# Optimization experiments

Hardware: AMD Instinct MI355X
Metric: run time of the kernel (lower is better)

The kernel has to match this reference:

```python
import jax, jax.numpy as jnp
import numpy as np

B, D_IN, D_H, W_RANK, U_RANK = 8192, 1024, 2048, 256, 256


def setup_inputs() -> dict:
    key = jax.random.key(0)
    ks = jax.random.split(key, 6)
    return {
        "input": jax.random.normal(ks[0], (B, D_IN), dtype=jnp.float32),
        "state": jax.random.normal(ks[1], (B, D_H), dtype=jnp.float32),
        "W1": 0.1 * jax.random.normal(ks[2], (W_RANK, D_IN), dtype=jnp.float32),
        "W2": 0.1 * jax.random.normal(ks[3], (D_H, W_RANK), dtype=jnp.float32),
        "U1": 0.1 * jax.random.normal(ks[4], (U_RANK, D_H), dtype=jnp.float32),
        "U2": 0.1 * jax.random.normal(ks[5], (D_H, U_RANK), dtype=jnp.float32),
        "bias_gate": jnp.ones((1, D_H), dtype=jnp.float32),
        "bias_update": jnp.ones((1, D_H), dtype=jnp.float32),
        "zeta": 1.0 * jnp.ones((1, 1), dtype=jnp.float32),
        "nu": -4.0 * jnp.ones((1, 1), dtype=jnp.float32),
    }


def reference(input, state, W1, W2, U1, U2, bias_gate, bias_update, zeta, nu):
    # Low-rank projections: Wx = x @ W1^T @ W2^T ; Uh = h @ U1^T @ U2^T
    wx = jnp.einsum("bi,ri->br", input, W1)          # [B, wRank]
    wx = jnp.einsum("br,hr->bh", wx, W2)             # [B, H]
    uh = jnp.einsum("bh,rh->br", state, U1)          # [B, uRank]
    uh = jnp.einsum("br,hr->bh", uh, U2)             # [B, H]
    pre = wx + uh                                     # shared pre-activation
    z = jax.nn.sigmoid(pre + bias_gate)               # gate (sigmoid)
    h_cand = jnp.tanh(pre + bias_update)              # update (tanh)
    # h_t = z*h_{t-1} + (sigmoid(zeta)*(1-z) + sigmoid(nu)) * h_cand
    new_h = z * state + (jax.nn.sigmoid(zeta) * (1.0 - z) + jax.nn.sigmoid(nu)) * h_cand
    return new_h
```

## Files before the change

kernel.cpp:

```cpp
#include <hip/hip_runtime.h>
#include <hip/hip_fp16.h>
#include <cstdint>
#include <cstddef>


typedef _Float16 half8 __attribute__((ext_vector_type(8)));
typedef float f32x4 __attribute__((ext_vector_type(4)));

#define DIN 1024
#define DH 2048
#define RK 256
#define RB6LD 1536
#define OFF_W1H 0
#define OFF_U1H 262144
#define OFF_W2H 786432
#define OFF_U2H 1310720
#define WB_HALVES 1835008

__device__ __forceinline__ half8 cvt8(const float4 a, const float4 b) {
  half8 h;
  h[0] = (_Float16)a.x; h[1] = (_Float16)a.y; h[2] = (_Float16)a.z; h[3] = (_Float16)a.w;
  h[4] = (_Float16)b.x; h[5] = (_Float16)b.y; h[6] = (_Float16)b.z; h[7] = (_Float16)b.w;
  return h;
}

__global__ __launch_bounds__(256)
void fgrnn_prep(const float* __restrict__ W1, const float* __restrict__ U1,
                const float* __restrict__ W2, const float* __restrict__ U2,
                _Float16* __restrict__ wb) {
  const int q = blockIdx.x * 256 + threadIdx.x;
  const float* src;
  int rel;
  if (q < 65536) { src = W1; rel = q; }
  else if (q < 196608) { src = U1; rel = q - 65536; }
  else if (q < 327680) { src = W2; rel = q - 196608; }
  else { src = U2; rel = q - 327680; }
  const float4 v = reinterpret_cast<const float4*>(src)[rel];
  union { _Float16 h[4]; uint2 u; } cv;
  cv.h[0] = (_Float16)v.x; cv.h[1] = (_Float16)v.y;
  cv.h[2] = (_Float16)v.z; cv.h[3] = (_Float16)v.w;
  reinterpret_cast<uint2*>(wb)[q] = cv.u;
}

__global__ __launch_bounds__(256)
void fgrnn_stage1(const float* __restrict__ x, const float* __restrict__ h,
                  const _Float16* __restrict__ wb, _Float16* __restrict__ rb6) {
  const int bid = blockIdx.x;
  const int L = (bid & 7) * 192 + (bid >> 3);
  const int p = L >> 8;
  const int rem = L & 255;
  const int ncol = rem >> 7;
  const int mtile = rem & 127;
  const bool isx = (p < 2);
  const float* A = isx ? x : h;
  const int KA = isx ? DIN : DH;
  const int kbase = (isx ? p : (p - 2)) * 512;
  const _Float16* Bw = wb + (isx ? OFF_W1H : OFF_U1H) + (size_t)(ncol * 128) * KA;
  const int row0 = mtile * 64;
  const int colbase = p * 256 + ncol * 128;

  __shared__ _Float16 As[64 * 64];
  __shared__ _Float16 Bs[128 * 64];

  const int tid = threadIdx.x;
  const int lane = tid & 63;
  const int w = tid >> 6;
  const int wr = w >> 1, wc = w & 1;

  f32x4 acc[2][4];
#pragma unroll
  for (int i = 0; i < 2; ++i)
#pragma unroll
    for (int j = 0; j < 4; ++j) acc[i][j] = (f32x4){0.f, 0.f, 0.f, 0.f};

  const int sr = tid >> 3;
  const int sc = (tid & 7) * 8;

  float4 pa4[2][2];
  half8 pb[4];

  auto LOADG = [&](int it) {
    const int k0 = kbase + it * 64;
#pragma unroll
    for (int j = 0; j < 2; ++j) {
      const float* s = A + (size_t)(row0 + j * 32 + sr) * KA + k0 + sc;
      pa4[j][0] = *reinterpret_cast<const float4*>(s);
      pa4[j][1] = *reinterpret_cast<const float4*>(s + 4);
    }
#pragma unroll
    for (int j = 0; j < 4; ++j)
      pb[j] = *reinterpret_cast<const half8*>(Bw + (size_t)(j * 32 + sr) * KA + k0 + sc);
  };
  auto STORE = [&]() {
#pragma unroll
    for (int j = 0; j < 2; ++j) {
      const int r = j * 32 + sr;
      *reinterpret_cast<half8*>(&As[r * 64 + (sc ^ ((r & 7) << 3))]) =
          cvt8(pa4[j][0], pa4[j][1]);
    }
#pragma unroll
    for (int j = 0; j < 4; ++j) {
      const int r = j * 32 + sr;
      *reinterpret_cast<half8*>(&Bs[r * 64 + (sc ^ ((r & 7) << 3))]) = pb[j];
    }
  };

  LOADG(0);
  STORE();
  __syncthreads();

  for (int it = 0; it < 8; ++it) {
    const bool more = (it + 1 < 8);
    if (more) LOADG(it + 1);
#pragma unroll
    for (int kk = 0; kk < 64; kk += 32) {
      half8 af[2], bf[4];
#pragma unroll
      for (int mi = 0; mi < 2; ++mi) {
        const int r = wr * 32 + mi * 16 + (lane & 15);
        af[mi] = *reinterpret_cast<const half8*>(
            &As[r * 64 + ((kk + 8 * (lane >> 4)) ^ ((r & 7) << 3))]);
      }
#pragma unroll
      for (int ni = 0; ni < 4; ++ni) {
        const int r = wc * 64 + ni * 16 + (lane & 15);
        bf[ni] = *reinterpret_cast<const half8*>(
            &Bs[r * 64 + ((kk + 8 * (lane >> 4)) ^ ((r & 7) << 3))]);
      }
#pragma unroll
      for (int mi = 0; mi < 2; ++mi)
#pragma unroll
        for (int ni = 0; ni < 4; ++ni)
          acc[mi][ni] =
              __builtin_amdgcn_mfma_f32_16x16x32_f16(af[mi], bf[ni], acc[mi][ni], 0, 0, 0);
    }
    if (more) {
      __syncthreads();
      STORE();
    }
    __syncthreads();
  }

#pragma unroll
  for (int mi = 0; mi < 2; ++mi)
#pragma unroll
    for (int ni = 0; ni < 4; ++ni)
#pragma unroll
      for (int e = 0; e < 4; ++e) {
        const int row = row0 + wr * 32 + mi * 16 + 4 * (lane >> 4) + e;
        const int col = colbase + wc * 64 + ni * 16 + (lane & 15);
        rb6[(size_t)row * RB6LD + col] = (_Float16)acc[mi][ni][e];
      }
}

__global__ __launch_bounds__(256)
void fgrnn_reduce(const _Float16* __restrict__ rb6, _Float16* __restrict__ rb2) {
  const int t = blockIdx.x * 256 + threadIdx.x;
  const int row = t >> 6;
  const int ch = t & 63;
  const _Float16* src = rb6 + (size_t)row * RB6LD;
  half8 s;
  int outcol;
  if (ch < 32) {
    const int c = ch * 8;
    s = *reinterpret_cast<const half8*>(src + c) +
        *reinterpret_cast<const half8*>(src + 256 + c);
    outcol = c;
  } else {
    const int c = (ch - 32) * 8;
    const _Float16* su = src + 512;
    s = *reinterpret_cast<const half8*>(su + c) +
        *reinterpret_cast<const half8*>(su + 256 + c);
    s = s + *reinterpret_cast<const half8*>(su + 512 + c);
    s = s + *reinterpret_cast<const half8*>(su + 768 + c);
    outcol = 256 + c;
  }
  *reinterpret_cast<half8*>(rb2 + (size_t)row * 512 + outcol) = s;
}

__global__ __launch_bounds__(256)
void fgrnn_stage2(const _Float16* __restrict__ rb2, const _Float16* __restrict__ wb,
                  const float* __restrict__ state,
                  const float* __restrict__ bg, const float* __restrict__ bu,
                  const float* __restrict__ zeta, const float* __restrict__ nu,
                  float* __restrict__ out) {
  const int bid = blockIdx.x;
  const int L = (bid & 7) * 256 + (bid >> 3);
  const int mtile = L >> 4;
  const int ntile = L & 15;
  const int row0 = mtile * 64;
  const int col0 = ntile * 128;
  const _Float16* W2h = wb + OFF_W2H;
  const _Float16* U2h = wb + OFF_U2H;

  __shared__ _Float16 As[64 * 64];
  __shared__ _Float16 Bs[128 * 64];

  const int tid = threadIdx.x;
  const int lane = tid & 63;
  const int w = tid >> 6;
  const int wr = w >> 1, wc = w & 1;

  f32x4 acc[2][4];
#pragma unroll
  for (int i = 0; i < 2; ++i)
#pragma unroll
    for (int j = 0; j < 4; ++j) acc[i][j] = (f32x4){0.f, 0.f, 0.f, 0.f};

  const int sr = tid >> 3;
  const int sc = (tid & 7) * 8;

  half8 pa[2], pb[4];

  auto LOADG = [&](int it) {
    const int k0 = it * 64;
#pragma unroll
    for (int j = 0; j < 2; ++j)
      pa[j] = *reinterpret_cast<const half8*>(rb2 + (size_t)(row0 + j * 32 + sr) * 512 + k0 + sc);
    const _Float16* Bh = (k0 < 256) ? W2h : U2h;
    const int kb = k0 & 255;
#pragma unroll
    for (int j = 0; j < 4; ++j)
      pb[j] = *reinterpret_cast<const half8*>(Bh + (size_t)(col0 + j * 32 + sr) * RK + kb + sc);
  };
  auto STORE = [&]() {
#pragma unroll
    for (int j = 0; j < 2; ++j) {
      const int r = j * 32 + sr;
      *reinterpret_cast<half8*>(&As[r * 64 + (sc ^ ((r & 7) << 3))]) = pa[j];
    }
#pragma unroll
    for (int j = 0; j < 4; ++j) {
      const int r = j * 32 + sr;
      *reinterpret_cast<half8*>(&Bs[r * 64 + (sc ^ ((r & 7) << 3))]) = pb[j];
    }
  };

  LOADG(0);
  STORE();
  __syncthreads();

  for (int it = 0; it < 8; ++it) {
    const bool more = (it + 1 < 8);
    if (more) LOADG(it + 1);
#pragma unroll
    for (int kk = 0; kk < 64; kk += 32) {
      half8 af[2], bf[4];
#pragma unroll
      for (int mi = 0; mi < 2; ++mi) {
        const int r = wr * 32 + mi * 16 + (lane & 15);
        af[mi] = *reinterpret_cast<const half8*>(
            &As[r * 64 + ((kk + 8 * (lane >> 4)) ^ ((r & 7) << 3))]);
      }
#pragma unroll
      for (int ni = 0; ni < 4; ++ni) {
        const int r = wc * 64 + ni * 16 + (lane & 15);
        bf[ni] = *reinterpret_cast<const half8*>(
            &Bs[r * 64 + ((kk + 8 * (lane >> 4)) ^ ((r & 7) << 3))]);
      }
#pragma unroll
      for (int mi = 0; mi < 2; ++mi)
#pragma unroll
        for (int ni = 0; ni < 4; ++ni)
          acc[mi][ni] =
              __builtin_amdgcn_mfma_f32_16x16x32_f16(af[mi], bf[ni], acc[mi][ni], 0, 0, 0);
    }
    if (more) {
      __syncthreads();
      STORE();
    }
    __syncthreads();
  }

  const float LOG2E = 1.44269504f;
  const float sz = __builtin_amdgcn_rcpf(1.f + __builtin_amdgcn_exp2f(-zeta[0] * LOG2E));
  const float sn = __builtin_amdgcn_rcpf(1.f + __builtin_amdgcn_exp2f(-nu[0] * LOG2E));
#pragma unroll
  for (int mi = 0; mi < 2; ++mi)
#pragma unroll
    for (int ni = 0; ni < 4; ++ni) {
      const int col = col0 + wc * 64 + ni * 16 + (lane & 15);
      const float bgc = bg[col];
      const float buc = bu[col];
#pragma unroll
      for (int e = 0; e < 4; ++e) {
        const int row = row0 + wr * 32 + mi * 16 + 4 * (lane >> 4) + e;
        const float pre = acc[mi][ni][e];
        const float zg =
            __builtin_amdgcn_rcpf(1.f + __builtin_amdgcn_exp2f(-(pre + bgc) * LOG2E));
        const float hc =
            1.f - 2.f * __builtin_amdgcn_rcpf(
                            1.f + __builtin_amdgcn_exp2f((pre + buc) * (2.f * LOG2E)));
        const float sv = state[(size_t)row * DH + col];
        out[(size_t)row * DH + col] = zg * sv + (sz * (1.f - zg) + sn) * hc;
      }
    }
}

extern "C" void kernel_launch(void* const* d_in, const int* in_sizes, int n_in,
                              void* d_out, int out_size, void* d_ws, size_t ws_size,
                              hipStream_t stream) {
  const float* input = (const float*)d_in[0];
  const float* state = (const float*)d_in[1];
  const float* W1 = (const float*)d_in[2];
  const float* W2 = (const float*)d_in[3];
  const float* U1 = (const float*)d_in[4];
  const float* U2 = (const float*)d_in[5];
  const float* bg = (const float*)d_in[6];
  const float* bu = (const float*)d_in[7];
  const float* zeta = (const float*)d_in[8];
  const float* nu = (const float*)d_in[9];
  float* out = (float*)d_out;

  _Float16* rb6 = (_Float16*)d_ws;
  _Float16* rb2 = rb6 + (size_t)8192 * RB6LD;
  _Float16* wb = rb2 + (size_t)8192 * 512;

  fgrnn_prep<<<1792, 256, 0, stream>>>(W1, U1, W2, U2, wb);
  fgrnn_stage1<<<1536, 256, 0, stream>>>(input, state, wb, rb6);
  fgrnn_reduce<<<2048, 256, 0, stream>>>(rb6, rb2);
  fgrnn_stage2<<<2048, 256, 0, stream>>>(rb2, wb, state, bg, bu, zeta, nu, out);
}
```

Before: 85.75 us.

## Use direct global-to-LDS loads with triple-buffered pipeline in stage1 GEMM

Stage1 now fetches A (fp32) and B (fp16) tiles straight into shared memory with global_load_lds, using three buffers and a K-step of 32 instead of a register-staged double buffer with K-step 64. The fp32-to-fp16 conversion of A moves from the store phase to the LDS-read phase inside compute. Waits use explicit vmcnt counts, and MFMA sections run at raised priority. The goal is to overlap memory latency with MFMA work and cut register pressure and barrier overhead. In exchange, A takes twice the LDS space and bandwidth as fp32, there are twice as many iterations, and the hand-counted vmcnt waits are fragile.

```diff
diff --git a/kernel.cpp b/kernel.cpp
--- a/kernel.cpp
+++ b/kernel.cpp
@@ -15,13 +15,24 @@
 #define OFF_U1H 262144
 #define OFF_W2H 786432
 #define OFF_U2H 1310720
-#define WB_HALVES 1835008
-
+
+__device__ __forceinline__ half8 cvt8f(f32x4 a, f32x4 b) {
+  half8 h;
+  h[0] = (_Float16)a[0]; h[1] = (_Float16)a[1]; h[2] = (_Float16)a[2]; h[3] = (_Float16)a[3];
+  h[4] = (_Float16)b[0]; h[5] = (_Float16)b[1]; h[6] = (_Float16)b[2]; h[7] = (_Float16)b[3];
+  return h;
+}
 __device__ __forceinline__ half8 cvt8(const float4 a, const float4 b) {
   half8 h;
   h[0] = (_Float16)a.x; h[1] = (_Float16)a.y; h[2] = (_Float16)a.z; h[3] = (_Float16)a.w;
   h[4] = (_Float16)b.x; h[5] = (_Float16)b.y; h[6] = (_Float16)b.z; h[7] = (_Float16)b.w;
   return h;
+}
+
+__device__ __forceinline__ void gload16(const void* g, void* lds) {
+  __builtin_amdgcn_global_load_lds(
+      (const __attribute__((address_space(1))) unsigned*)g,
+      (__attribute__((address_space(3))) unsigned*)lds, 16, 0, 0);
 }
 
 __global__ __launch_bounds__(256)
@@ -45,6 +56,9 @@
 __global__ __launch_bounds__(256)
 void fgrnn_stage1(const float* __restrict__ x, const float* __restrict__ h,
                   const _Float16* __restrict__ wb, _Float16* __restrict__ rb6) {
+  __shared__ float Af[3][64 * 32];
+  __shared__ _Float16 Bf[3][128 * 32];
+
   const int bid = blockIdx.x;
   const int L = (bid & 7) * 192 + (bid >> 3);
   const int p = L >> 8;
@@ -59,13 +73,10 @@
   const int row0 = mtile * 64;
   const int colbase = p * 256 + ncol * 128;
 
-  __shared__ _Float16 As[64 * 64];
-  __shared__ _Float16 Bs[128 * 64];
-
   const int tid = threadIdx.x;
   const int lane = tid & 63;
-  const int w = tid >> 6;
-  const int wr = w >> 1, wc = w & 1;
+  const int wv = tid >> 6;
+  const int wr = wv >> 1, wc = wv & 1;
 
   f32x4 acc[2][4];
 #pragma unroll
@@ -73,72 +84,72 @@
 #pragma unroll
     for (int j = 0; j < 4; ++j) acc[i][j] = (f32x4){0.f, 0.f, 0.f, 0.f};
 
-  const int sr = tid >> 3;
-  const int sc = (tid & 7) * 8;
-
-  float4 pa4[2][2];
-  half8 pb[4];
-
-  auto LOADG = [&](int it) {
-    const int k0 = kbase + it * 64;
-#pragma unroll
-    for (int j = 0; j < 2; ++j) {
-      const float* s = A + (size_t)(row0 + j * 32 + sr) * KA + k0 + sc;
-      pa4[j][0] = *reinterpret_cast<const float4*>(s);
-      pa4[j][1] = *reinterpret_cast<const float4*>(s + 4);
-    }
-#pragma unroll
-    for (int j = 0; j < 4; ++j)
-      pb[j] = *reinterpret_cast<const half8*>(Bw + (size_t)(j * 32 + sr) * KA + k0 + sc);
+  const int aRowL = (lane >> 3);
+  const int aCh = (lane & 7) ^ aRowL;
+  const int bRowL = (lane >> 2);
+  const int bCh = (lane & 3) ^ (lane >> 4);
+
+  auto GLOAD = [&](int buf, int it) {
+    const int k0 = kbase + it * 32;
+#pragma unroll
+    for (int g = 0; g < 2; ++g) {
+      const int rb = wv * 16 + g * 8;
+      gload16(A + (size_t)(row0 + rb + aRowL) * KA + k0 + aCh * 4,
+              &Af[buf][rb * 32]);
+    }
+#pragma unroll
+    for (int g = 0; g < 2; ++g) {
+      const int rb = wv * 32 + g * 16;
+      gload16(Bw + (size_t)(rb + bRowL) * KA + k0 + bCh * 8,
+              &Bf[buf][rb * 32]);
+    }
   };
-  auto STORE = [&]() {
-#pragma unroll
-    for (int j = 0; j < 2; ++j) {
-      const int r = j * 32 + sr;
-      *reinterpret_cast<half8*>(&As[r * 64 + (sc ^ ((r & 7) << 3))]) =
-          cvt8(pa4[j][0], pa4[j][1]);
-    }
-#pragma unroll
-    for (int j = 0; j < 4; ++j) {
-      const int r = j * 32 + sr;
-      *reinterpret_cast<half8*>(&Bs[r * 64 + (sc ^ ((r & 7) << 3))]) = pb[j];
-    }
+
+  auto COMPUTE = [&](int buf) {
+    half8 af[2], bf[4];
+    const int g = lane >> 4;
+#pragma unroll
+    for (int mi = 0; mi < 2; ++mi) {
+      const int r = wr * 32 + mi * 16 + (lane & 15);
+      const int c0 = (2 * g) ^ (r & 7);
+      const int c1 = (2 * g + 1) ^ (r & 7);
+      const f32x4 lo = *reinterpret_cast<const f32x4*>(&Af[buf][r * 32 + c0 * 4]);
+      const f32x4 hi = *reinterpret_cast<const f32x4*>(&Af[buf][r * 32 + c1 * 4]);
+      af[mi] = cvt8f(lo, hi);
+    }
+#pragma unroll
+    for (int ni = 0; ni < 4; ++ni) {
+      const int r = wc * 64 + ni * 16 + (lane & 15);
+      const int c = g ^ ((r >> 2) & 3);
+      bf[ni] = *reinterpret_cast<const half8*>(&Bf[buf][r * 32 + c * 8]);
+    }
+#pragma unroll
+    for (int mi = 0; mi < 2; ++mi)
+#pragma unroll
+      for (int ni = 0; ni < 4; ++ni)
+        acc[mi][ni] =
+            __builtin_amdgcn_mfma_f32_16x16x32_f16(af[mi], bf[ni], acc[mi][ni], 0, 0, 0);
   };
 
-  LOADG(0);
-  STORE();
-  __syncthreads();
-
-  for (int it = 0; it < 8; ++it) {
-    const bool more = (it + 1 < 8);
-    if (more) LOADG(it + 1);
-#pragma unroll
-    for (int kk = 0; kk < 64; kk += 32) {
-      half8 af[2], bf[4];
-#pragma unroll
-      for (int mi = 0; mi < 2; ++mi) {
-        const int r = wr * 32 + mi * 16 + (lane & 15);
-        af[mi] = *reinterpret_cast<const half8*>(
-            &As[r * 64 + ((kk + 8 * (lane >> 4)) ^ ((r & 7) << 3))]);
-      }
-#pragma unroll
-      for (int ni = 0; ni < 4; ++ni) {
-        const int r = wc * 64 + ni * 16 + (lane & 15);
-        bf[ni] = *reinterpret_cast<const half8*>(
-            &Bs[r * 64 + ((kk + 8 * (lane >> 4)) ^ ((r & 7) << 3))]);
-      }
-#pragma unroll
-      for (int mi = 0; mi < 2; ++mi)
-#pragma unroll
-        for (int ni = 0; ni < 4; ++ni)
-          acc[mi][ni] =
-              __builtin_amdgcn_mfma_f32_16x16x32_f16(af[mi], bf[ni], acc[mi][ni], 0, 0, 0);
-    }
-    if (more) {
-      __syncthreads();
-      STORE();
-    }
-    __syncthreads();
+  GLOAD(0, 0);
+  GLOAD(1, 1);
+  asm volatile("s_waitcnt vmcnt(4)" ::: "memory");
+  __builtin_amdgcn_s_barrier();
+  __builtin_amdgcn_sched_barrier(0);
+
+#pragma unroll
+  for (int t = 0; t < 16; ++t) {
+    if (t + 2 < 16) GLOAD((t + 2) % 3, t + 2);
+    __builtin_amdgcn_s_setprio(1);
+    COMPUTE(t % 3);
+    __builtin_amdgcn_s_setprio(0);
+    if (t + 2 < 16) {
+      asm volatile("s_waitcnt vmcnt(4)" ::: "memory");
+    } else if (t + 1 < 16) {
+      asm volatile("s_waitcnt vmcnt(0)" ::: "memory");
+    }
+    __builtin_amdgcn_s_barrier();
+    __builtin_amdgcn_sched_barrier(0);
   }
 
 #pragma unroll
```

Result: no change. 85.96 us (+0.2%).

## Preload whole A row-panel into LDS and double-buffer B tiles in stage1

Applied to the files above, without the earlier changes.

Stage1 now uses 32-row M tiles instead of 64, doubling the grid to 3072 blocks. Each block converts its full 32x512 A slice to fp16 in LDS up front, and only the B tiles are streamed through a double-buffered LDS pipeline. The aim is more parallelism and less per-iteration global traffic and conversion work for A. In exchange, each B tile is reloaded by twice as many blocks, each wave does half as much MFMA work per B fragment read, and LDS use per block grows to about 64KB, which may cap occupancy.

```diff
diff --git a/kernel.cpp b/kernel.cpp
--- a/kernel.cpp
+++ b/kernel.cpp
@@ -15,7 +15,6 @@
 #define OFF_U1H 262144
 #define OFF_W2H 786432
 #define OFF_U2H 1310720
-#define WB_HALVES 1835008
 
 __device__ __forceinline__ half8 cvt8(const float4 a, const float4 b) {
   half8 h;
@@ -45,112 +44,102 @@
 __global__ __launch_bounds__(256)
 void fgrnn_stage1(const float* __restrict__ x, const float* __restrict__ h,
                   const _Float16* __restrict__ wb, _Float16* __restrict__ rb6) {
+  __shared__ _Float16 Ap[32 * 512];
+  __shared__ _Float16 Bs[2][128 * 64];
+
   const int bid = blockIdx.x;
-  const int L = (bid & 7) * 192 + (bid >> 3);
-  const int p = L >> 8;
-  const int rem = L & 255;
-  const int ncol = rem >> 7;
-  const int mtile = rem & 127;
+  const int L = (bid & 7) * 384 + (bid >> 3);
+  const int p = L / 512;
+  const int rem = L & 511;
+  const int ncol = rem >> 8;
+  const int mtile = rem & 255;
   const bool isx = (p < 2);
   const float* A = isx ? x : h;
   const int KA = isx ? DIN : DH;
   const int kbase = (isx ? p : (p - 2)) * 512;
   const _Float16* Bw = wb + (isx ? OFF_W1H : OFF_U1H) + (size_t)(ncol * 128) * KA;
-  const int row0 = mtile * 64;
+  const int row0 = mtile * 32;
   const int colbase = p * 256 + ncol * 128;
-
-  __shared__ _Float16 As[64 * 64];
-  __shared__ _Float16 Bs[128 * 64];
 
   const int tid = threadIdx.x;
   const int lane = tid & 63;
-  const int w = tid >> 6;
-  const int wr = w >> 1, wc = w & 1;
-
-  f32x4 acc[2][4];
-#pragma unroll
-  for (int i = 0; i < 2; ++i)
-#pragma unroll
-    for (int j = 0; j < 4; ++j) acc[i][j] = (f32x4){0.f, 0.f, 0.f, 0.f};
+  const int wv = tid >> 6;
+  const int wr = wv >> 1, wc = wv & 1;
+
+  {
+    const int ar = tid >> 3;
+    const int ac0 = (tid & 7) * 8;
+    const float* src = A + (size_t)(row0 + ar) * KA + kbase;
+#pragma unroll
+    for (int pass = 0; pass < 8; ++pass) {
+      const int c = ac0 + pass * 64;
+      const float4 v0 = *reinterpret_cast<const float4*>(src + c);
+      const float4 v1 = *reinterpret_cast<const float4*>(src + c + 4);
+      const int ch = (c >> 3) ^ (ar & 7);
+      *reinterpret_cast<half8*>(&Ap[ar * 512 + ch * 8]) = cvt8(v0, v1);
+    }
+  }
 
   const int sr = tid >> 3;
   const int sc = (tid & 7) * 8;
-
-  float4 pa4[2][2];
   half8 pb[4];
-
-  auto LOADG = [&](int it) {
+  auto LOADB = [&](int it) {
     const int k0 = kbase + it * 64;
-#pragma unroll
-    for (int j = 0; j < 2; ++j) {
-      const float* s = A + (size_t)(row0 + j * 32 + sr) * KA + k0 + sc;
-      pa4[j][0] = *reinterpret_cast<const float4*>(s);
-      pa4[j][1] = *reinterpret_cast<const float4*>(s + 4);
-    }
 #pragma unroll
     for (int j = 0; j < 4; ++j)
       pb[j] = *reinterpret_cast<const half8*>(Bw + (size_t)(j * 32 + sr) * KA + k0 + sc);
   };
-  auto STORE = [&]() {
-#pragma unroll
-    for (int j = 0; j < 2; ++j) {
-      const int r = j * 32 + sr;
-      *reinterpret_cast<half8*>(&As[r * 64 + (sc ^ ((r & 7) << 3))]) =
-          cvt8(pa4[j][0], pa4[j][1]);
-    }
+  auto STOREB = [&](int buf) {
 #pragma unroll
     for (int j = 0; j < 4; ++j) {
       const int r = j * 32 + sr;
-      *reinterpret_cast<half8*>(&Bs[r * 64 + (sc ^ ((r & 7) << 3))]) = pb[j];
+      *reinterpret_cast<half8*>(&Bs[buf][r * 64 + (sc ^ ((r & 7) << 3))]) = pb[j];
     }
   };
 
-  LOADG(0);
-  STORE();
+  f32x4 acc[4];
+#pragma unroll
+  for (int j = 0; j < 4; ++j) acc[j] = (f32x4){0.f, 0.f, 0.f, 0.f};
+
+  LOADB(0);
+  STOREB(0);
   __syncthreads();
 
   for (int it = 0; it < 8; ++it) {
     const bool more = (it + 1 < 8);
-    if (more) LOADG(it + 1);
+    const int buf = it & 1;
+    if (more) LOADB(it + 1);
 #pragma unroll
     for (int kk = 0; kk < 64; kk += 32) {
-      half8 af[2], bf[4];
-#pragma unroll
-      for (int mi = 0; mi < 2; ++mi) {
-        const int r = wr * 32 + mi * 16 + (lane & 15);
-        af[mi] = *reinterpret_cast<const half8*>(
-            &As[r * 64 + ((kk + 8 * (lane >> 4)) ^ ((r & 7) << 3))]);
+      const int r = wr * 16 + (lane & 15);
+      const int chA = (it * 8 + (kk >> 3) + (lane >> 4)) ^ (r & 7);
+      const half8 af = *reinterpret_cast<const half8*>(&Ap[r * 512 + chA * 8]);
+      half8 bf[4];
+#pragma unroll
+      for (int ni = 0; ni < 4; ++ni) {
+        const int rb_ = wc * 64 + ni * 16 + (lane & 15);
+        bf[ni] = *reinterpret_cast<const half8*>(
+            &Bs[buf][rb_ * 64 + ((kk + 8 * (lane >> 4)) ^ ((rb_ & 7) << 3))]);
       }
 #pragma unroll
-      for (int ni = 0; ni < 4; ++ni) {
-        const int r = wc * 64 + ni * 16 + (lane & 15);
-        bf[ni] = *reinterpret_cast<const half8*>(
-            &Bs[r * 64 + ((kk + 8 * (lane >> 4)) ^ ((r & 7) << 3))]);
-      }
-#pragma unroll
-      for (int mi = 0; mi < 2; ++mi)
-#pragma unroll
-        for (int ni = 0; ni < 4; ++ni)
-          acc[mi][ni] =
-              __builtin_amdgcn_mfma_f32_16x16x32_f16(af[mi], bf[ni], acc[mi][ni], 0, 0, 0);
+      for (int ni = 0; ni < 4; ++ni)
+        acc[ni] = __builtin_amdgcn_mfma_f32_16x16x32_f16(af, bf[ni], acc[ni], 0, 0, 0);
     }
     if (more) {
       __syncthreads();
-      STORE();
+      STOREB(buf ^ 1);
     }
     __syncthreads();
   }
 
 #pragma unroll
-  for (int mi = 0; mi < 2; ++mi)
-#pragma unroll
-    for (int ni = 0; ni < 4; ++ni)
-#pragma unroll
-      for (int e = 0; e < 4; ++e) {
-        const int row = row0 + wr * 32 + mi * 16 + 4 * (lane >> 4) + e;
-        const int col = colbase + wc * 64 + ni * 16 + (lane & 15);
-        rb6[(size_t)row * RB6LD + col] = (_Float16)acc[mi][ni][e];
-      }
+  for (int ni = 0; ni < 4; ++ni)
+#pragma unroll
+    for (int e = 0; e < 4; ++e) {
+      const int row = row0 + wr * 16 + 4 * (lane >> 4) + e;
+      const int col = colbase + wc * 64 + ni * 16 + (lane & 15);
+      rb6[(size_t)row * RB6LD + col] = (_Float16)acc[ni][e];
+    }
 }
 
 __global__ __launch_bounds__(256)
@@ -317,7 +306,7 @@
   _Float16* wb = rb2 + (size_t)8192 * 512;
 
   fgrnn_prep<<<1792, 256, 0, stream>>>(W1, U1, W2, U2, wb);
-  fgrnn_stage1<<<1536, 256, 0, stream>>>(input, state, wb, rb6);
+  fgrnn_stage1<<<3072, 256, 0, stream>>>(input, state, wb, rb6);
   fgrnn_reduce<<<2048, 256, 0, stream>>>(rb6, rb2);
   fgrnn_stage2<<<2048, 256, 0, stream>>>(rb2, wb, state, bg, bu, zeta, nu, out);
 }
```

Measured after the change: 104.6 us. 22.0% more time.
